# Optimization experiments

Hardware: AMD Instinct MI355X
Metric: run time of the kernel (lower is better)

## Reference

```python
import jax, jax.numpy as jnp
import numpy as np

N_COMPONENTS = 256
GAMMA = 1.0
TWO_PI = 6.283185307179586

def setup_inputs() -> dict:
    key = jax.random.key(0)
    k1, k2, k3, k4, k5 = jax.random.split(key, 5)
    B, D, OUT = 262144, 64, 18
    x = jax.random.normal(k1, (B, D), dtype=jnp.float32)
    # RBFSampler: random_weights_ = sqrt(2*gamma) * N(0,1), shape (D, n_components)
    W_rbf = jax.random.normal(k2, (D, N_COMPONENTS), dtype=jnp.float32)
    # random_offset_ = Uniform(0, 2*pi)
    b_rbf = jax.random.uniform(k3, (N_COMPONENTS,), dtype=jnp.float32)
    W_lin = jax.random.normal(k4, (OUT, N_COMPONENTS), dtype=jnp.float32) * (1.0 / np.sqrt(N_COMPONENTS))
    b_lin = jax.random.normal(k5, (OUT,), dtype=jnp.float32) * 0.01
    return {"x": x, "W_rbf": W_rbf, "b_rbf": b_rbf, "W_lin": W_lin, "b_lin": b_lin}

def reference(x, W_rbf, b_rbf, W_lin, b_lin):
    # RBF random-feature map (sklearn RBFSampler, gamma=1):
    # z = sqrt(2/n_components) * cos(x @ (sqrt(2*gamma)*W) + 2*pi*b)
    proj = x @ (jnp.sqrt(2.0 * GAMMA) * W_rbf) + TWO_PI * b_rbf  # [B, 256]
    feat = jnp.cos(proj) * jnp.sqrt(2.0 / N_COMPONENTS)          # [B, 256]
    # Linear head: feat @ W_lin.T + b_lin
    return feat @ W_lin.T + b_lin                                 # [B, 18]
```

## Files before the change

### kernel.cpp

```cpp
#include <hip/hip_runtime.h>
#include <cstdint>
#include <cstddef>

typedef __attribute__((ext_vector_type(8))) short bf16x8;
typedef __attribute__((ext_vector_type(8))) _Float16 f16x8;
typedef __attribute__((ext_vector_type(4))) float f32x4;
typedef __attribute__((ext_vector_type(2))) float f32x2;
typedef __attribute__((ext_vector_type(2))) unsigned int u32x2;

static constexpr int BROWS  = 262144;
static constexpr int DIM    = 64;
static constexpr int NC     = 256;
static constexpr int OUTD   = 18;
static constexpr int BM     = 32;
static constexpr int NCHTOT = BROWS / BM;
static constexpr int NBLK   = 768;

__device__ __forceinline__ unsigned cvt_pk_bf16(float a, float b) {
  unsigned r;
  asm("v_cvt_pk_bf16_f32 %0, %1, %2" : "=v"(r) : "v"(a), "v"(b));
  return r;
}

union U4 { unsigned u[4]; bf16x8 v; };

__device__ __forceinline__ bf16x8 pack8(const float* s) {
  U4 r;
#pragma unroll
  for (int p = 0; p < 4; ++p) r.u[p] = cvt_pk_bf16(s[2*p], s[2*p+1]);
  return r.v;
}

__global__ __launch_bounds__(512, 4) void rbf_fused(
    const float* __restrict__ x,  const float* __restrict__ Wr,
    const float* __restrict__ br, const float* __restrict__ Wl,
    const float* __restrict__ bl, float* __restrict__ out)
{
  __shared__ __align__(16) unsigned short xh16[2][BM * DIM];
  __shared__ __align__(16) unsigned short featb[2][BM * NC];
  __shared__ __align__(16) unsigned short wlds[OUTD * NC];

  const int tid  = threadIdx.x;
  const int wav  = tid >> 6;
  const int lane = tid & 63;
  const int li   = lane & 15;
  const int g    = lane >> 4;

  const float S1 = 0.22507907903927651f;
  const float SC = 0.08838834764831845f;

  for (int idx = tid; idx < OUTD * 32; idx += 512) {
    const int r = idx >> 5, c = idx & 31;
    f32x4 v0 = *(const f32x4*)(Wl + r*NC + 8*c);
    f32x4 v1 = *(const f32x4*)(Wl + r*NC + 8*c + 4);
    float v[8];
    v[0]=v0.x; v[1]=v0.y; v[2]=v0.z; v[3]=v0.w;
    v[4]=v1.x; v[5]=v1.y; v[6]=v1.z; v[7]=v1.w;
    *(bf16x8*)(&wlds[r*NC + 8*(c ^ (r & 7))]) = pack8(v);
  }

  f16x8 a1[2][2];
#pragma unroll
  for (int q = 0; q < 2; ++q) {
    const int n = 16 * (2*wav + q) + li;
#pragma unroll
    for (int kb = 0; kb < 2; ++kb) {
      f16x8 f;
#pragma unroll
      for (int j = 0; j < 8; ++j)
        f[j] = (_Float16)(Wr[(size_t)(32*kb + 8*g + j) * NC + n] * S1);
      a1[q][kb] = f;
    }
  }
  f32x4 brf[2];
#pragma unroll
  for (int q = 0; q < 2; ++q)
    brf[q] = *(const f32x4*)(br + 16*(2*wav + q) + 4*g);

  const f32x4 bl0 = *(const f32x4*)(bl + 4*g);
  const float bl16 = bl[16], bl17 = bl[17];
  const int rowc = (li < 2) ? (16 + li) : li;

  const int sr = tid >> 4;
  const int g4 = tid & 15;

  auto stage_write = [&](int p, f32x4 v) {
    union { _Float16 h[4]; u32x2 u; } cv;
    cv.h[0] = (_Float16)v.x; cv.h[1] = (_Float16)v.y;
    cv.h[2] = (_Float16)v.z; cv.h[3] = (_Float16)v.w;
    const int offs = sr*DIM + 8*((g4 >> 1) ^ (sr & 7)) + 4*(g4 & 1);
    *(u32x2*)(&xh16[p][offs]) = cv.u;
  };

  {
    const float* xp = x + ((size_t)blockIdx.x * BM + sr) * DIM + 4*g4;
    stage_write(0, *(const f32x4*)xp);
  }
  asm volatile("s_waitcnt lgkmcnt(0)" ::: "memory");
  __builtin_amdgcn_s_barrier();
  asm volatile("" ::: "memory");

  int pb = 0;
  for (int c = blockIdx.x; c < NCHTOT; c += NBLK, pb ^= 1) {
    const int R = c * BM;

    f32x4 pnext;
    const bool havenext = (c + NBLK < NCHTOT);
    if (havenext) {
      const float* xp = x + ((size_t)(c + NBLK) * BM + sr) * DIM + 4*g4;
      pnext = *(const f32x4*)xp;
    }

#pragma unroll
    for (int rt = 0; rt < 2; ++rt) {
      const int rr = rt*16 + li;
      const int m  = li & 7;
      f16x8 bh[2];
#pragma unroll
      for (int kb = 0; kb < 2; ++kb) {
        const int slot = 8*((4*kb + g) ^ m);
        bh[kb] = *(const f16x8*)(&xh16[pb][rr*DIM + slot]);
      }
      f32x4 acc[2];
#pragma unroll
      for (int q = 0; q < 2; ++q) acc[q] = f32x4{0.f, 0.f, 0.f, 0.f};
#pragma unroll
      for (int kb = 0; kb < 2; ++kb) {
#pragma unroll
        for (int q = 0; q < 2; ++q)
          acc[q] = __builtin_amdgcn_mfma_f32_16x16x32_f16(a1[q][kb], bh[kb], acc[q], 0, 0, 0);
      }
#pragma unroll
      for (int q = 0; q < 2; ++q) {
        float c4[4];
#pragma unroll
        for (int j = 0; j < 4; ++j) {
          float rev = acc[q][j] + brf[q][j];
          float f   = rev - floorf(rev);
          c4[j] = __builtin_amdgcn_cosf(f) * SC;
        }
        u32x2 pk;
        pk.x = cvt_pk_bf16(c4[0], c4[1]);
        pk.y = cvt_pk_bf16(c4[2], c4[3]);
        const int nt   = 2*wav + q;
        const int slot = (2*nt + (g >> 1)) ^ m;
        *(u32x2*)(&featb[pb][rr*256 + slot*8 + (g & 1)*4]) = pk;
      }
    }

    if (havenext) stage_write(pb ^ 1, pnext);

    asm volatile("s_waitcnt lgkmcnt(0)" ::: "memory");
    __builtin_amdgcn_s_barrier();
    asm volatile("" ::: "memory");

    if (wav < 4) {
      const int rt2 = wav & 1;
      const int ot  = wav >> 1;
      const int rr  = rt2*16 + li;
      const int m   = li & 7;
      const int arow = (ot == 0) ? li : rowc;
      const int asw  = arow & 7;
      f32x4 acc2 = f32x4{0.f,0.f,0.f,0.f};
#pragma unroll
      for (int kb = 0; kb < 8; ++kb) {
        bf16x8 b2  = *(const bf16x8*)(&featb[pb][rr*256 + (((4*kb + g) ^ m) * 8)]);
        bf16x8 a2f = *(const bf16x8*)(&wlds[arow*NC + 8*((4*kb + g) ^ asw)]);
        acc2 = __builtin_amdgcn_mfma_f32_16x16x32_bf16(a2f, b2, acc2, 0, 0, 0);
      }
      float* op = out + (size_t)(R + rr) * OUTD;
      if (ot == 0) {
        f32x2 s0; s0.x = acc2.x + bl0.x; s0.y = acc2.y + bl0.y;
        f32x2 s1; s1.x = acc2.z + bl0.z; s1.y = acc2.w + bl0.w;
        *(f32x2*)(op + 4*g)     = s0;
        *(f32x2*)(op + 4*g + 2) = s1;
      } else if (g == 0) {
        f32x2 s2; s2.x = acc2.x + bl16; s2.y = acc2.y + bl17;
        *(f32x2*)(op + 16) = s2;
      }
    }
  }
}

extern "C" void kernel_launch(void* const* d_in, const int* in_sizes, int n_in,
                              void* d_out, int out_size, void* d_ws, size_t ws_size,
                              hipStream_t stream) {
  (void)in_sizes; (void)n_in; (void)d_ws; (void)ws_size; (void)out_size;
  const float* x  = (const float*)d_in[0];
  const float* Wr = (const float*)d_in[1];
  const float* br = (const float*)d_in[2];
  const float* Wl = (const float*)d_in[3];
  const float* bl = (const float*)d_in[4];
  rbf_fused<<<NBLK, 512, 0, stream>>>(x, Wr, br, Wl, bl, (float*)d_out);
}
```

Baseline: 31.35 us.

## Load x directly from global into MFMA operands and prepack W_lin via separate kernel

Drops the LDS double-buffered staging of x. Each wave now loads its x rows straight from global memory and converts them to fp16 in registers before the first MFMA. W_lin is packed to bf16 once by a small pre-kernel into a global buffer, and the second GEMM reads it from there instead of from LDS. This cuts per-block LDS usage and prologue work, which allows the grid to grow to 1024 blocks. The costs are an extra kernel launch, redundant global reads of x by several waves, and losing the prefetch overlap of the next chunk.

```diff
diff --git a/kernel.cpp b/kernel.cpp
--- a/kernel.cpp
+++ b/kernel.cpp
@@ -14,7 +14,7 @@
 static constexpr int OUTD   = 18;
 static constexpr int BM     = 32;
 static constexpr int NCHTOT = BROWS / BM;
-static constexpr int NBLK   = 768;
+static constexpr int NBLK   = 1024;
 
 __device__ __forceinline__ unsigned cvt_pk_bf16(float a, float b) {
   unsigned r;
@@ -31,14 +31,26 @@
   return r.v;
 }
 
+__device__ __align__(16) unsigned short g_wpack[OUTD * NC];
+
+__global__ void pack_wl(const float* __restrict__ Wl) {
+  for (int idx = threadIdx.x; idx < OUTD * 32; idx += 512) {
+    const int r = idx >> 5, c = idx & 31;
+    f32x4 v0 = *(const f32x4*)(Wl + r*NC + 8*c);
+    f32x4 v1 = *(const f32x4*)(Wl + r*NC + 8*c + 4);
+    float v[8];
+    v[0]=v0.x; v[1]=v0.y; v[2]=v0.z; v[3]=v0.w;
+    v[4]=v1.x; v[5]=v1.y; v[6]=v1.z; v[7]=v1.w;
+    *(bf16x8*)(&g_wpack[r*NC + 8*c]) = pack8(v);
+  }
+}
+
 __global__ __launch_bounds__(512, 4) void rbf_fused(
     const float* __restrict__ x,  const float* __restrict__ Wr,
-    const float* __restrict__ br, const float* __restrict__ Wl,
-    const float* __restrict__ bl, float* __restrict__ out)
+    const float* __restrict__ br, const float* __restrict__ bl,
+    float* __restrict__ out)
 {
-  __shared__ __align__(16) unsigned short xh16[2][BM * DIM];
   __shared__ __align__(16) unsigned short featb[2][BM * NC];
-  __shared__ __align__(16) unsigned short wlds[OUTD * NC];
 
   const int tid  = threadIdx.x;
   const int wav  = tid >> 6;
@@ -48,16 +60,6 @@
 
   const float S1 = 0.22507907903927651f;
   const float SC = 0.08838834764831845f;
-
-  for (int idx = tid; idx < OUTD * 32; idx += 512) {
-    const int r = idx >> 5, c = idx & 31;
-    f32x4 v0 = *(const f32x4*)(Wl + r*NC + 8*c);
-    f32x4 v1 = *(const f32x4*)(Wl + r*NC + 8*c + 4);
-    float v[8];
-    v[0]=v0.x; v[1]=v0.y; v[2]=v0.z; v[3]=v0.w;
-    v[4]=v1.x; v[5]=v1.y; v[6]=v1.z; v[7]=v1.w;
-    *(bf16x8*)(&wlds[r*NC + 8*(c ^ (r & 7))]) = pack8(v);
-  }
 
   f16x8 a1[2][2];
 #pragma unroll
@@ -81,45 +83,31 @@
   const float bl16 = bl[16], bl17 = bl[17];
   const int rowc = (li < 2) ? (16 + li) : li;
 
-  const int sr = tid >> 4;
-  const int g4 = tid & 15;
-
-  auto stage_write = [&](int p, f32x4 v) {
-    union { _Float16 h[4]; u32x2 u; } cv;
-    cv.h[0] = (_Float16)v.x; cv.h[1] = (_Float16)v.y;
-    cv.h[2] = (_Float16)v.z; cv.h[3] = (_Float16)v.w;
-    const int offs = sr*DIM + 8*((g4 >> 1) ^ (sr & 7)) + 4*(g4 & 1);
-    *(u32x2*)(&xh16[p][offs]) = cv.u;
-  };
-
-  {
-    const float* xp = x + ((size_t)blockIdx.x * BM + sr) * DIM + 4*g4;
-    stage_write(0, *(const f32x4*)xp);
-  }
-  asm volatile("s_waitcnt lgkmcnt(0)" ::: "memory");
-  __builtin_amdgcn_s_barrier();
-  asm volatile("" ::: "memory");
+  const int rt2p = wav & 1;
+  const int otp  = wav >> 1;
+  const int arow = (otp == 0) ? li : rowc;
 
   int pb = 0;
   for (int c = blockIdx.x; c < NCHTOT; c += NBLK, pb ^= 1) {
     const int R = c * BM;
-
-    f32x4 pnext;
-    const bool havenext = (c + NBLK < NCHTOT);
-    if (havenext) {
-      const float* xp = x + ((size_t)(c + NBLK) * BM + sr) * DIM + 4*g4;
-      pnext = *(const f32x4*)xp;
-    }
+    const float* xg = x + (size_t)R * DIM;
 
 #pragma unroll
     for (int rt = 0; rt < 2; ++rt) {
       const int rr = rt*16 + li;
       const int m  = li & 7;
+      const float* xp = xg + rr*DIM;
       f16x8 bh[2];
 #pragma unroll
       for (int kb = 0; kb < 2; ++kb) {
-        const int slot = 8*((4*kb + g) ^ m);
-        bh[kb] = *(const f16x8*)(&xh16[pb][rr*DIM + slot]);
+        f32x4 p0 = *(const f32x4*)(xp + 32*kb + 8*g);
+        f32x4 p1 = *(const f32x4*)(xp + 32*kb + 8*g + 4);
+        union { _Float16 h[8]; f16x8 v; } cv;
+        cv.h[0]=(_Float16)p0.x; cv.h[1]=(_Float16)p0.y;
+        cv.h[2]=(_Float16)p0.z; cv.h[3]=(_Float16)p0.w;
+        cv.h[4]=(_Float16)p1.x; cv.h[5]=(_Float16)p1.y;
+        cv.h[6]=(_Float16)p1.z; cv.h[7]=(_Float16)p1.w;
+        bh[kb] = cv.v;
       }
       f32x4 acc[2];
 #pragma unroll
@@ -148,28 +136,24 @@
       }
     }
 
-    if (havenext) stage_write(pb ^ 1, pnext);
-
     asm volatile("s_waitcnt lgkmcnt(0)" ::: "memory");
     __builtin_amdgcn_s_barrier();
     asm volatile("" ::: "memory");
 
     if (wav < 4) {
-      const int rt2 = wav & 1;
-      const int ot  = wav >> 1;
-      const int rr  = rt2*16 + li;
-      const int m   = li & 7;
-      const int arow = (ot == 0) ? li : rowc;
-      const int asw  = arow & 7;
+      const unsigned short* wp = &g_wpack[0];
+      asm volatile("" : "+v"(wp));
+      const int rr = rt2p*16 + li;
+      const int m  = li & 7;
       f32x4 acc2 = f32x4{0.f,0.f,0.f,0.f};
 #pragma unroll
       for (int kb = 0; kb < 8; ++kb) {
         bf16x8 b2  = *(const bf16x8*)(&featb[pb][rr*256 + (((4*kb + g) ^ m) * 8)]);
-        bf16x8 a2f = *(const bf16x8*)(&wlds[arow*NC + 8*((4*kb + g) ^ asw)]);
-        acc2 = __builtin_amdgcn_mfma_f32_16x16x32_bf16(a2f, b2, acc2, 0, 0, 0);
+        bf16x8 a2k = *(const bf16x8*)(wp + arow*NC + 32*kb + 8*g);
+        acc2 = __builtin_amdgcn_mfma_f32_16x16x32_bf16(a2k, b2, acc2, 0, 0, 0);
       }
       float* op = out + (size_t)(R + rr) * OUTD;
-      if (ot == 0) {
+      if (otp == 0) {
         f32x2 s0; s0.x = acc2.x + bl0.x; s0.y = acc2.y + bl0.y;
         f32x2 s1; s1.x = acc2.z + bl0.z; s1.y = acc2.w + bl0.w;
         *(f32x2*)(op + 4*g)     = s0;
@@ -191,5 +175,6 @@
   const float* br = (const float*)d_in[2];
   const float* Wl = (const float*)d_in[3];
   const float* bl = (const float*)d_in[4];
-  rbf_fused<<<NBLK, 512, 0, stream>>>(x, Wr, br, Wl, bl, (float*)d_out);
+  pack_wl<<<1, 512, 0, stream>>>(Wl);
+  rbf_fused<<<NBLK, 512, 0, stream>>>(x, Wr, br, bl, (float*)d_out);
 }
```

Result: slower. 100.2 us (+219.4%).
